# Kernel optimization log

Hardware: AMD Instinct MI355X
Metric: run time of the kernel (lower is better)

## Reference

```python
import jax, jax.numpy as jnp
import numpy as np

EPS = 1e-5          # BatchNorm eps
SG_ALPHA = 4.0      # spikingjelly sigmoid surrogate alpha
NUM_EXPERTS = 8
TOP_K = 2
ROUTER_TAU = 2.0
TAUS = tuple(1.5 + (4.0 - 1.5) * i / (NUM_EXPERTS - 1) for i in range(NUM_EXPERTS))

@jax.custom_vjp
def spike(x):
    # Heaviside(x >= 0) with sigmoid surrogate gradient
    return (x >= 0).astype(x.dtype)

def _spike_fwd(x):
    return spike(x), x

def _spike_bwd(x, g):
    s = jax.nn.sigmoid(SG_ALPHA * x)
    return (g * SG_ALPHA * s * (1.0 - s),)

spike.defvjp(_spike_fwd, _spike_bwd)

def conv1x1(x, w, b):
    # x: (N,C,H,W), w: (O,C) 1x1 conv kernel, b: (O,)
    return jnp.einsum('nchw,oc->nohw', x, w) + b[None, :, None, None]

def bn(x, gamma, beta):
    # fresh BatchNorm2d inference: running_mean=0, running_var=1
    scale = gamma / np.float32(np.sqrt(1.0 + EPS))
    return x * scale[None, :, None, None] + beta[None, :, None, None]

def setup_inputs() -> dict:
    key = jax.random.key(0)
    ks = jax.random.split(key, 16)
    T, B, C, H, W = 4, 64, 64, 32, 32
    E = NUM_EXPERTS
    inp = {
        'x':  jax.random.normal(ks[0], (T, B, C, H, W), jnp.float32) * 2.0,
        'w1': jax.random.normal(ks[1], (E, C, C), jnp.float32) * 0.05,
        'b1': jax.random.normal(ks[2], (E, C), jnp.float32) * 0.05,
        'g1': jax.random.uniform(ks[3], (E, C), jnp.float32, 0.5, 1.5),
        'be1': jax.random.normal(ks[4], (E, C), jnp.float32) * 0.05,
        'w2': jax.random.normal(ks[5], (E, C, C), jnp.float32) * 0.05,
        'b2': jax.random.normal(ks[6], (E, C), jnp.float32) * 0.05,
        'g2': jax.random.uniform(ks[7], (E, C), jnp.float32, 0.5, 1.5),
        'be2': jax.random.normal(ks[8], (E, C), jnp.float32) * 0.05,
        'rw': jax.random.normal(ks[9], (E, C), jnp.float32) * 0.05,
        'rb': jax.random.normal(ks[10], (E,), jnp.float32) * 0.05,
        'rg': jax.random.uniform(ks[11], (E,), jnp.float32, 0.5, 1.5),
        'rbe': jax.random.normal(ks[12], (E,), jnp.float32) * 0.05,
    }
    return inp

def reference(x, w1, b1, g1, be1, w2, b2, g2, be2, rw, rb, rg, rbe):
    T, B, C, H, W = x.shape
    N = T * B
    # ---- Router: multi-step LIF over T, then 1x1 conv + BN + spatial mean ----
    def lif_step(v, xt):
        v = v + (xt - v) / ROUTER_TAU
        s = spike(v - 1.0)
        v = v * (1.0 - jax.lax.stop_gradient(s))  # detach_reset, hard reset to 0
        return v, s
    _, spk = jax.lax.scan(lif_step, jnp.zeros_like(x[0]), x)  # (T,B,C,H,W)
    r = bn(conv1x1(spk.reshape(N, C, H, W), rw, rb), rg, rbe)  # (N,E,H,W)
    logits = r.mean(axis=(2, 3))                               # (N,E)
    probs = jax.nn.softmax(logits, axis=-1)
    wk, idx = jax.lax.top_k(probs, TOP_K)                      # (N,k)
    wk = wk / wk.sum(axis=-1, keepdims=True)
    wk = jax.lax.stop_gradient(wk)                             # weights detached
    # dense combine weights: weight of expert e for each token (0 if unselected)
    combine = jnp.zeros((N, NUM_EXPERTS), x.dtype).at[jnp.arange(N)[:, None], idx].add(wk)
    # ---- Experts: each token processed independently (T=1, fresh LIF state) ----
    xf = x.reshape(N, C, H, W)
    out = jnp.zeros_like(xf)
    for e in range(NUM_EXPERTS):
        tau = TAUS[e]
        s1 = spike(xf / tau - 1.0)                 # single-step LIF: v=x/tau, thresh 1
        h = bn(conv1x1(s1, w1[e], b1[e]), g1[e], be1[e])
        x2 = xf + h                                # res=True (hidden == in_features)
        s2 = spike(x2 / tau - 1.0)
        y = bn(conv1x1(s2, w2[e], b2[e]), g2[e], be2[e])
        eo = y + x2                                # expert's own residual
        out = out + combine[:, e, None, None, None] * eo
    return (out + xf).reshape(T, B, C, H, W)       # final identity add
```

## Files before the change

kernel.cpp:

```cpp
#include <hip/hip_runtime.h>
#include <hip/hip_bf16.h>

#define TT 4
#define BB 64
#define CC 64
#define PP 1024
#define NN 256
#define EE 8

#define RSQ 0.99999500003749975f

typedef __attribute__((ext_vector_type(8))) short short8;
typedef __attribute__((ext_vector_type(4))) float f32x4;

static __device__ __forceinline__ float rfl_f(float v) {
    return __uint_as_float(__builtin_amdgcn_readfirstlane(__float_as_uint(v)));
}
static __device__ __forceinline__ unsigned short f2bf(float v) {
    __hip_bfloat16 h = __float2bfloat16(v);
    return *reinterpret_cast<unsigned short*>(&h);
}

__global__ void k_lif_prep(const float* __restrict__ x, float* __restrict__ mean_spk,
                           const float* __restrict__ w1, const float* __restrict__ b1,
                           const float* __restrict__ g1, const float* __restrict__ be1,
                           const float* __restrict__ w2, const float* __restrict__ b2,
                           const float* __restrict__ g2, const float* __restrict__ be2,
                           unsigned short* __restrict__ wb,
                           float* __restrict__ fb1, float* __restrict__ fb2) {
    if (blockIdx.x >= BB * CC) {
        int idx = (blockIdx.x - BB * CC) * 256 + threadIdx.x;
        if (idx < EE * CC * CC) {
            int e = idx >> 12, rem = idx & 4095;
            int o = rem >> 6;
            float s1 = g1[e * 64 + o] * RSQ;
            float s2 = g2[e * 64 + o] * RSQ;
            wb[(e * 2 + 0) * 4096 + rem] = f2bf(w1[idx] * s1);
            wb[(e * 2 + 1) * 4096 + rem] = f2bf(w2[idx] * s2);
        }
        if (idx < EE * CC) {
            fb1[idx] = b1[idx] * (g1[idx] * RSQ) + be1[idx];
            fb2[idx] = b2[idx] * (g2[idx] * RSQ) + be2[idx];
        }
        return;
    }
    int bc = blockIdx.x;
    int b = bc >> 6, c = bc & 63;
    int tid = threadIdx.x;
    const size_t tstride = (size_t)BB * CC * PP;
    const float* xp = x + ((size_t)b * CC + c) * PP + tid * 4;
    f32x4 v = {0.f, 0.f, 0.f, 0.f};
    float cnt[4];
    #pragma unroll
    for (int t = 0; t < 4; ++t) {
        f32x4 xt = *(const f32x4*)(xp + t * tstride);
        float cc = 0.f;
        #pragma unroll
        for (int r = 0; r < 4; ++r) {
            v[r] += (xt[r] - v[r]) * 0.5f;
            bool s = v[r] >= 1.f;
            cc += s ? 1.f : 0.f;
            v[r] = s ? 0.f : v[r];
        }
        cnt[t] = cc;
    }
    __shared__ float red[4][4];
    int lane = tid & 63, wv = tid >> 6;
    #pragma unroll
    for (int off = 32; off > 0; off >>= 1) {
        cnt[0] += __shfl_down(cnt[0], off, 64);
        cnt[1] += __shfl_down(cnt[1], off, 64);
        cnt[2] += __shfl_down(cnt[2], off, 64);
        cnt[3] += __shfl_down(cnt[3], off, 64);
    }
    if (lane == 0) { red[wv][0] = cnt[0]; red[wv][1] = cnt[1]; red[wv][2] = cnt[2]; red[wv][3] = cnt[3]; }
    __syncthreads();
    if (tid < 4) {
        float s = red[0][tid] + red[1][tid] + red[2][tid] + red[3][tid];
        mean_spk[((size_t)tid * BB + b) * CC + c] = s * (1.f / 1024.f);
    }
}

template <int BIT>
static __device__ __forceinline__ short8 unpack8(unsigned d0, unsigned d1) {
    const unsigned am = 0x00010001u << BIT;
    const unsigned mu = 0x3F80u >> BIT;
    union { unsigned u[4]; short8 s; } cv;
    unsigned t;
    t = __builtin_amdgcn_perm(0u, d0, 0x0C010C00u) & am; cv.u[0] = t * mu;
    t = __builtin_amdgcn_perm(0u, d0, 0x0C030C02u) & am; cv.u[1] = t * mu;
    t = __builtin_amdgcn_perm(0u, d1, 0x0C010C00u) & am; cv.u[2] = t * mu;
    t = __builtin_amdgcn_perm(0u, d1, 0x0C030C02u) & am; cv.u[3] = t * mu;
    return cv.s;
}

__global__ void __launch_bounds__(256) __attribute__((amdgpu_waves_per_eu(4, 8))) k_experts(
    const float* __restrict__ x, const float* __restrict__ mean_spk,
    const float* __restrict__ rw, const float* __restrict__ rb,
    const float* __restrict__ rg, const float* __restrict__ rbe,
    const unsigned short* __restrict__ wb,
    const float* __restrict__ fb1, const float* __restrict__ fb2,
    float* __restrict__ out)
{
    __shared__ unsigned char s1[2][64 * 72];
    __shared__ unsigned char s2[2][64 * 72];

    int blk = blockIdx.x;
    int n = blk >> 2;
    int q = blk & 3;
    int tid = threadIdx.x;
    int z = tid >> 6;
    int lane = tid & 63;
    int l16 = lane & 15;
    int g = lane >> 4;
    int Q0 = q << 8;
    int ch = z * 16 + l16;

    const float* __restrict__ xn = x + (size_t)n * (CC * PP);

    int re = lane >> 3, rcb = (lane & 7) << 3;
    f32x4 msv0 = *(const f32x4*)(mean_spk + n * CC + rcb);
    f32x4 msv1 = *(const f32x4*)(mean_spk + n * CC + rcb + 4);
    f32x4 rwv0 = *(const f32x4*)(rw + re * CC + rcb);
    f32x4 rwv1 = *(const f32x4*)(rw + re * CC + rcb + 4);

    f32x4 xsbuf[2][4];
    {
        const float* xc = xn + (size_t)ch * PP + Q0 + 4 * g;
        #pragma unroll
        for (int tm = 0; tm < 4; ++tm)
            xsbuf[0][tm] = *(const f32x4*)(xc + tm * 16);
    }

    float part = 0.f;
    #pragma unroll
    for (int r = 0; r < 4; ++r) part = fmaf(msv0[r], rwv0[r], part);
    #pragma unroll
    for (int r = 0; r < 4; ++r) part = fmaf(msv1[r], rwv1[r], part);
    part += __shfl_xor(part, 1, 64);
    part += __shfl_xor(part, 2, 64);
    part += __shfl_xor(part, 4, 64);
    float logit = (part + rb[re]) * (rg[re] * RSQ) + rbe[re];
    float l[EE];
    #pragma unroll
    for (int j = 0; j < EE; ++j) l[j] = __shfl(logit, j << 3, 64);
    float m = l[0];
    #pragma unroll
    for (int e = 1; e < EE; ++e) m = fmaxf(m, l[e]);
    float pr[EE];
    #pragma unroll
    for (int e = 0; e < EE; ++e) pr[e] = __expf(l[e] - m);
    int e1i = 0; float v1 = pr[0];
    #pragma unroll
    for (int e = 1; e < EE; ++e) { if (pr[e] > v1) { v1 = pr[e]; e1i = e; } }
    int e2i = (e1i == 0) ? 1 : 0; float v2 = (e1i == 0) ? pr[1] : pr[0];
    #pragma unroll
    for (int e = 0; e < EE; ++e) { if (e != e1i && pr[e] > v2) { v2 = pr[e]; e2i = e; } }
    float wAv = v1 / (v1 + v2), wBv = v2 / (v1 + v2);

    int e1 = __builtin_amdgcn_readfirstlane(e1i);
    int e2 = __builtin_amdgcn_readfirstlane(e2i);
    wAv = rfl_f(wAv); wBv = rfl_f(wBv);
    float tauA = (float)(1.5 + 2.5 * (double)e1 / 7.0);
    float tauB = (float)(1.5 + 2.5 * (double)e2 / 7.0);
    float kx = (1.f + wAv + wBv) / wAv;

    const unsigned short* wbA = wb + e1 * 8192;
    const unsigned short* wbB = wb + e2 * 8192;

    short8 w1A[2], w1B[2], w2A[2], w2B[2];
    #pragma unroll
    for (int ks = 0; ks < 2; ++ks) {
        int wo = ch * 64 + ks * 32 + g * 8;
        w1A[ks] = *(const short8*)(wbA + wo);
        w1B[ks] = *(const short8*)(wbB + wo);
        w2A[ks] = *(const short8*)(wbA + 4096 + wo);
        w2B[ks] = *(const short8*)(wbB + 4096 + wo);
    }
    float b1A = fb1[e1 * 64 + ch];
    float b1B = fb1[e2 * 64 + ch];
    float cst = wAv * fb2[e1 * 64 + ch] + wBv * fb2[e2 * 64 + ch];

    #pragma unroll
    for (int tm = 0; tm < 4; ++tm)
        #pragma unroll
        for (int r = 0; r < 4; ++r) {
            float xv = xsbuf[0][tm][r];
            s1[0][(tm * 16 + 4 * g + r) * 72 + ch] =
                (unsigned char)((xv >= tauA ? 1u : 0u) | (xv >= tauB ? 2u : 0u));
        }
    __syncthreads();

    float* __restrict__ on = out + (size_t)n * (CC * PP);

    #pragma unroll
    for (int s = 0; s < 4; ++s) {
        const int par = s & 1, nxt = par ^ 1;

        if (s < 3) {
            const float* xc = xn + (size_t)ch * PP + Q0 + (s + 1) * 64 + 4 * g;
            #pragma unroll
            for (int tm = 0; tm < 4; ++tm)
                xsbuf[nxt][tm] = *(const f32x4*)(xc + tm * 16);
        }

        f32x4 accA[4], accB[4];
        #pragma unroll
        for (int tm = 0; tm < 4; ++tm) {
            accA[tm] = (f32x4){0.f, 0.f, 0.f, 0.f};
            accB[tm] = (f32x4){0.f, 0.f, 0.f, 0.f};
        }
        #pragma unroll
        for (int ks = 0; ks < 2; ++ks)
            #pragma unroll
            for (int tm = 0; tm < 4; ++tm) {
                const unsigned* mp = (const unsigned*)(&s1[par][0] + (tm * 16 + l16) * 72 + ks * 32 + g * 8);
                unsigned d0 = mp[0], d1 = mp[1];
                short8 aA = unpack8<0>(d0, d1);
                accA[tm] = __builtin_amdgcn_mfma_f32_16x16x32_bf16(aA, w1A[ks], accA[tm], 0, 0, 0);
                short8 aB = unpack8<1>(d0, d1);
                accB[tm] = __builtin_amdgcn_mfma_f32_16x16x32_bf16(aB, w1B[ks], accB[tm], 0, 0, 0);
            }

        #pragma unroll
        for (int tm = 0; tm < 4; ++tm)
            #pragma unroll
            for (int r = 0; r < 4; ++r) {
                float xv = xsbuf[par][tm][r];
                float bnA = accA[tm][r] + b1A;
                float bnB = accB[tm][r] + b1B;
                s2[par][(tm * 16 + 4 * g + r) * 72 + ch] =
                    (unsigned char)(((xv + bnA) >= tauA ? 1u : 0u) | ((xv + bnB) >= tauB ? 2u : 0u));
                accA[tm][r] = fmaf(xv, kx, bnA);
                accB[tm][r] = bnB;
            }

        if (s < 3) {
            #pragma unroll
            for (int tm = 0; tm < 4; ++tm)
                #pragma unroll
                for (int r = 0; r < 4; ++r) {
                    float xv = xsbuf[nxt][tm][r];
                    s1[nxt][(tm * 16 + 4 * g + r) * 72 + ch] =
                        (unsigned char)((xv >= tauA ? 1u : 0u) | (xv >= tauB ? 2u : 0u));
                }
        }
        __syncthreads();

        #pragma unroll
        for (int ks = 0; ks < 2; ++ks)
            #pragma unroll
            for (int tm = 0; tm < 4; ++tm) {
                const unsigned* mp = (const unsigned*)(&s2[par][0] + (tm * 16 + l16) * 72 + ks * 32 + g * 8);
                unsigned d0 = mp[0], d1 = mp[1];
                short8 aA = unpack8<0>(d0, d1);
                accA[tm] = __builtin_amdgcn_mfma_f32_16x16x32_bf16(aA, w2A[ks], accA[tm], 0, 0, 0);
                short8 aB = unpack8<1>(d0, d1);
                accB[tm] = __builtin_amdgcn_mfma_f32_16x16x32_bf16(aB, w2B[ks], accB[tm], 0, 0, 0);
            }

        #pragma unroll
        for (int tm = 0; tm < 4; ++tm) {
            f32x4 o;
            #pragma unroll
            for (int r = 0; r < 4; ++r)
                o[r] = fmaf(wAv, accA[tm][r], fmaf(wBv, accB[tm][r], cst));
            *(f32x4*)(on + (size_t)ch * PP + Q0 + s * 64 + tm * 16 + 4 * g) = o;
        }
    }
}

extern "C" void kernel_launch(void* const* d_in, const int* in_sizes, int n_in,
                              void* d_out, int out_size, void* d_ws, size_t ws_size,
                              hipStream_t stream) {
    const float* x   = (const float*)d_in[0];
    const float* w1  = (const float*)d_in[1];
    const float* b1  = (const float*)d_in[2];
    const float* g1  = (const float*)d_in[3];
    const float* be1 = (const float*)d_in[4];
    const float* w2  = (const float*)d_in[5];
    const float* b2  = (const float*)d_in[6];
    const float* g2  = (const float*)d_in[7];
    const float* be2 = (const float*)d_in[8];
    const float* rw  = (const float*)d_in[9];
    const float* rb  = (const float*)d_in[10];
    const float* rg  = (const float*)d_in[11];
    const float* rbe = (const float*)d_in[12];
    float* out = (float*)d_out;
    float* ws  = (float*)d_ws;

    float* mean_spk     = ws;
    unsigned short* wb  = (unsigned short*)(ws + 16384);
    float* fb1          = ws + 49152;
    float* fb2          = ws + 49664;

    hipLaunchKernelGGL(k_lif_prep, dim3(BB * CC + 128), dim3(256), 0, stream,
                       x, mean_spk, w1, b1, g1, be1, w2, b2, g2, be2, wb, fb1, fb2);
    hipLaunchKernelGGL(k_experts, dim3(NN * 4), dim3(256), 0, stream,
                       x, mean_spk, rw, rb, rg, rbe, wb, fb1, fb2, out);
}
```

Before: 48.70 us.

## Store spike masks as bf16 in LDS instead of packed bytes

Spike masks now go into shared memory as bf16 values (0 or 1.0) in separate per-expert planes, where before they were packed bits in bytes. The MFMA operands are then loaded directly as short8 with no perm/and/mul unpacking. Bias b1 is folded into the accumulator init, and an extra barrier is added because the s1 and s2 buffers are no longer double-buffered per stage. In exchange the LDS footprint and store traffic double per element, and the extra barrier adds synchronisation in each stage.

```diff
diff --git a/kernel.cpp b/kernel.cpp
--- a/kernel.cpp
+++ b/kernel.cpp
@@ -81,19 +81,6 @@
     }
 }
 
-template <int BIT>
-static __device__ __forceinline__ short8 unpack8(unsigned d0, unsigned d1) {
-    const unsigned am = 0x00010001u << BIT;
-    const unsigned mu = 0x3F80u >> BIT;
-    union { unsigned u[4]; short8 s; } cv;
-    unsigned t;
-    t = __builtin_amdgcn_perm(0u, d0, 0x0C010C00u) & am; cv.u[0] = t * mu;
-    t = __builtin_amdgcn_perm(0u, d0, 0x0C030C02u) & am; cv.u[1] = t * mu;
-    t = __builtin_amdgcn_perm(0u, d1, 0x0C010C00u) & am; cv.u[2] = t * mu;
-    t = __builtin_amdgcn_perm(0u, d1, 0x0C030C02u) & am; cv.u[3] = t * mu;
-    return cv.s;
-}
-
 __global__ void __launch_bounds__(256) __attribute__((amdgpu_waves_per_eu(4, 8))) k_experts(
     const float* __restrict__ x, const float* __restrict__ mean_spk,
     const float* __restrict__ rw, const float* __restrict__ rb,
@@ -102,8 +89,8 @@
     const float* __restrict__ fb1, const float* __restrict__ fb2,
     float* __restrict__ out)
 {
-    __shared__ unsigned char s1[2][64 * 72];
-    __shared__ unsigned char s2[2][64 * 72];
+    __shared__ unsigned short s1p[2][64 * 72];
+    __shared__ unsigned short s2p[2][64 * 72];
 
     int blk = blockIdx.x;
     int n = blk >> 2;
@@ -186,8 +173,9 @@
         #pragma unroll
         for (int r = 0; r < 4; ++r) {
             float xv = xsbuf[0][tm][r];
-            s1[0][(tm * 16 + 4 * g + r) * 72 + ch] =
-                (unsigned char)((xv >= tauA ? 1u : 0u) | (xv >= tauB ? 2u : 0u));
+            int px = tm * 16 + 4 * g + r;
+            s1p[0][px * 72 + ch] = (xv >= tauA) ? (unsigned short)0x3F80 : (unsigned short)0;
+            s1p[1][px * 72 + ch] = (xv >= tauB) ? (unsigned short)0x3F80 : (unsigned short)0;
         }
     __syncthreads();
 
@@ -207,32 +195,32 @@
         f32x4 accA[4], accB[4];
         #pragma unroll
         for (int tm = 0; tm < 4; ++tm) {
-            accA[tm] = (f32x4){0.f, 0.f, 0.f, 0.f};
-            accB[tm] = (f32x4){0.f, 0.f, 0.f, 0.f};
+            accA[tm] = (f32x4){b1A, b1A, b1A, b1A};
+            accB[tm] = (f32x4){b1B, b1B, b1B, b1B};
         }
         #pragma unroll
         for (int ks = 0; ks < 2; ++ks)
             #pragma unroll
             for (int tm = 0; tm < 4; ++tm) {
-                const unsigned* mp = (const unsigned*)(&s1[par][0] + (tm * 16 + l16) * 72 + ks * 32 + g * 8);
-                unsigned d0 = mp[0], d1 = mp[1];
-                short8 aA = unpack8<0>(d0, d1);
+                const unsigned short* rowp = &s1p[0][(tm * 16 + l16) * 72 + ks * 32 + g * 8];
+                short8 aA = *(const short8*)rowp;
+                short8 aB = *(const short8*)(rowp + 64 * 72);
                 accA[tm] = __builtin_amdgcn_mfma_f32_16x16x32_bf16(aA, w1A[ks], accA[tm], 0, 0, 0);
-                short8 aB = unpack8<1>(d0, d1);
                 accB[tm] = __builtin_amdgcn_mfma_f32_16x16x32_bf16(aB, w1B[ks], accB[tm], 0, 0, 0);
             }
+        __syncthreads();
 
         #pragma unroll
         for (int tm = 0; tm < 4; ++tm)
             #pragma unroll
             for (int r = 0; r < 4; ++r) {
                 float xv = xsbuf[par][tm][r];
-                float bnA = accA[tm][r] + b1A;
-                float bnB = accB[tm][r] + b1B;
-                s2[par][(tm * 16 + 4 * g + r) * 72 + ch] =
-                    (unsigned char)(((xv + bnA) >= tauA ? 1u : 0u) | ((xv + bnB) >= tauB ? 2u : 0u));
+                float bnA = accA[tm][r];
+                float bnB = accB[tm][r];
+                int px = tm * 16 + 4 * g + r;
+                s2p[0][px * 72 + ch] = ((xv + bnA) >= tauA) ? (unsigned short)0x3F80 : (unsigned short)0;
+                s2p[1][px * 72 + ch] = ((xv + bnB) >= tauB) ? (unsigned short)0x3F80 : (unsigned short)0;
                 accA[tm][r] = fmaf(xv, kx, bnA);
-                accB[tm][r] = bnB;
             }
 
         if (s < 3) {
@@ -241,8 +229,9 @@
                 #pragma unroll
                 for (int r = 0; r < 4; ++r) {
                     float xv = xsbuf[nxt][tm][r];
-                    s1[nxt][(tm * 16 + 4 * g + r) * 72 + ch] =
-                        (unsigned char)((xv >= tauA ? 1u : 0u) | (xv >= tauB ? 2u : 0u));
+                    int px = tm * 16 + 4 * g + r;
+                    s1p[0][px * 72 + ch] = (xv >= tauA) ? (unsigned short)0x3F80 : (unsigned short)0;
+                    s1p[1][px * 72 + ch] = (xv >= tauB) ? (unsigned short)0x3F80 : (unsigned short)0;
                 }
         }
         __syncthreads();
@@ -251,11 +240,10 @@
         for (int ks = 0; ks < 2; ++ks)
             #pragma unroll
             for (int tm = 0; tm < 4; ++tm) {
-                const unsigned* mp = (const unsigned*)(&s2[par][0] + (tm * 16 + l16) * 72 + ks * 32 + g * 8);
-                unsigned d0 = mp[0], d1 = mp[1];
-                short8 aA = unpack8<0>(d0, d1);
+                const unsigned short* rowp = &s2p[0][(tm * 16 + l16) * 72 + ks * 32 + g * 8];
+                short8 aA = *(const short8*)rowp;
+                short8 aB = *(const short8*)(rowp + 64 * 72);
                 accA[tm] = __builtin_amdgcn_mfma_f32_16x16x32_bf16(aA, w2A[ks], accA[tm], 0, 0, 0);
-                short8 aB = unpack8<1>(d0, d1);
                 accB[tm] = __builtin_amdgcn_mfma_f32_16x16x32_bf16(aB, w2B[ks], accB[tm], 0, 0, 0);
             }
 
```

After: 46.71 us (median of 2 runs). 1.04x faster.

## Fuse LIF router prep and expert phase into one cooperative kernel with grid sync

Applied to the files above, without the earlier changes.

Merges the LIF/weight-prep kernel and the expert kernel into a single cooperative launch of 1024 blocks. Each block first does four (b,c) LIF reductions plus a share of weight prep, then waits at a grid-wide sync before running the expert phase. This removes a kernel launch and the gap between the two kernels. The cost is a grid barrier, and the launch falls back to two kernels if the grid cannot be co-resident. The change also drops the LDS double buffering in favour of single buffers with an extra __syncthreads, and folds b1 into the accumulator initialisation.

```diff
diff --git a/kernel.cpp b/kernel.cpp
--- a/kernel.cpp
+++ b/kernel.cpp
@@ -1,5 +1,6 @@
 #include <hip/hip_runtime.h>
 #include <hip/hip_bf16.h>
+#include <hip/hip_cooperative_groups.h>
 
 #define TT 4
 #define BB 64
@@ -13,12 +14,27 @@
 typedef __attribute__((ext_vector_type(8))) short short8;
 typedef __attribute__((ext_vector_type(4))) float f32x4;
 
+namespace cg = cooperative_groups;
+
 static __device__ __forceinline__ float rfl_f(float v) {
     return __uint_as_float(__builtin_amdgcn_readfirstlane(__float_as_uint(v)));
 }
 static __device__ __forceinline__ unsigned short f2bf(float v) {
     __hip_bfloat16 h = __float2bfloat16(v);
     return *reinterpret_cast<unsigned short*>(&h);
+}
+
+template <int BIT>
+static __device__ __forceinline__ short8 unpack8(unsigned d0, unsigned d1) {
+    const unsigned am = 0x00010001u << BIT;
+    const unsigned mu = 0x3F80u >> BIT;
+    union { unsigned u[4]; short8 s; } cv;
+    unsigned t;
+    t = __builtin_amdgcn_perm(0u, d0, 0x0C010C00u) & am; cv.u[0] = t * mu;
+    t = __builtin_amdgcn_perm(0u, d0, 0x0C030C02u) & am; cv.u[1] = t * mu;
+    t = __builtin_amdgcn_perm(0u, d1, 0x0C010C00u) & am; cv.u[2] = t * mu;
+    t = __builtin_amdgcn_perm(0u, d1, 0x0C030C02u) & am; cv.u[3] = t * mu;
+    return cv.s;
 }
 
 __global__ void k_lif_prep(const float* __restrict__ x, float* __restrict__ mean_spk,
@@ -81,17 +97,177 @@
     }
 }
 
-template <int BIT>
-static __device__ __forceinline__ short8 unpack8(unsigned d0, unsigned d1) {
-    const unsigned am = 0x00010001u << BIT;
-    const unsigned mu = 0x3F80u >> BIT;
-    union { unsigned u[4]; short8 s; } cv;
-    unsigned t;
-    t = __builtin_amdgcn_perm(0u, d0, 0x0C010C00u) & am; cv.u[0] = t * mu;
-    t = __builtin_amdgcn_perm(0u, d0, 0x0C030C02u) & am; cv.u[1] = t * mu;
-    t = __builtin_amdgcn_perm(0u, d1, 0x0C010C00u) & am; cv.u[2] = t * mu;
-    t = __builtin_amdgcn_perm(0u, d1, 0x0C030C02u) & am; cv.u[3] = t * mu;
-    return cv.s;
+static __device__ __forceinline__ void expert_phase(
+    int blk, int tid,
+    const float* __restrict__ x, const float* __restrict__ mean_spk,
+    const float* __restrict__ rw, const float* __restrict__ rb,
+    const float* __restrict__ rg, const float* __restrict__ rbe,
+    const unsigned short* __restrict__ wb,
+    const float* __restrict__ fb1, const float* __restrict__ fb2,
+    float* __restrict__ out,
+    unsigned char* __restrict__ s1, unsigned char* __restrict__ s2)
+{
+    int n = blk >> 2;
+    int q = blk & 3;
+    int z = tid >> 6;
+    int lane = tid & 63;
+    int l16 = lane & 15;
+    int g = lane >> 4;
+    int Q0 = q << 8;
+    int ch = z * 16 + l16;
+
+    const float* __restrict__ xn = x + (size_t)n * (CC * PP);
+
+    int re = lane >> 3, rcb = (lane & 7) << 3;
+    f32x4 msv0 = *(const f32x4*)(mean_spk + n * CC + rcb);
+    f32x4 msv1 = *(const f32x4*)(mean_spk + n * CC + rcb + 4);
+    f32x4 rwv0 = *(const f32x4*)(rw + re * CC + rcb);
+    f32x4 rwv1 = *(const f32x4*)(rw + re * CC + rcb + 4);
+
+    f32x4 xsbuf[2][4];
+    {
+        const float* xc = xn + (size_t)ch * PP + Q0 + 4 * g;
+        #pragma unroll
+        for (int tm = 0; tm < 4; ++tm)
+            xsbuf[0][tm] = *(const f32x4*)(xc + tm * 16);
+    }
+
+    float part = 0.f;
+    #pragma unroll
+    for (int r = 0; r < 4; ++r) part = fmaf(msv0[r], rwv0[r], part);
+    #pragma unroll
+    for (int r = 0; r < 4; ++r) part = fmaf(msv1[r], rwv1[r], part);
+    part += __shfl_xor(part, 1, 64);
+    part += __shfl_xor(part, 2, 64);
+    part += __shfl_xor(part, 4, 64);
+    float logit = (part + rb[re]) * (rg[re] * RSQ) + rbe[re];
+    float l[EE];
+    #pragma unroll
+    for (int j = 0; j < EE; ++j) l[j] = __shfl(logit, j << 3, 64);
+    float m = l[0];
+    #pragma unroll
+    for (int e = 1; e < EE; ++e) m = fmaxf(m, l[e]);
+    float pr[EE];
+    #pragma unroll
+    for (int e = 0; e < EE; ++e) pr[e] = __expf(l[e] - m);
+    int e1i = 0; float v1 = pr[0];
+    #pragma unroll
+    for (int e = 1; e < EE; ++e) { if (pr[e] > v1) { v1 = pr[e]; e1i = e; } }
+    int e2i = (e1i == 0) ? 1 : 0; float v2 = (e1i == 0) ? pr[1] : pr[0];
+    #pragma unroll
+    for (int e = 0; e < EE; ++e) { if (e != e1i && pr[e] > v2) { v2 = pr[e]; e2i = e; } }
+    float wAv = v1 / (v1 + v2), wBv = v2 / (v1 + v2);
+
+    int e1 = __builtin_amdgcn_readfirstlane(e1i);
+    int e2 = __builtin_amdgcn_readfirstlane(e2i);
+    wAv = rfl_f(wAv); wBv = rfl_f(wBv);
+    float tauA = (float)(1.5 + 2.5 * (double)e1 / 7.0);
+    float tauB = (float)(1.5 + 2.5 * (double)e2 / 7.0);
+    float kx = (1.f + wAv + wBv) / wAv;
+
+    const unsigned short* wbA = wb + e1 * 8192;
+    const unsigned short* wbB = wb + e2 * 8192;
+
+    short8 w1A[2], w1B[2], w2A[2], w2B[2];
+    #pragma unroll
+    for (int ks = 0; ks < 2; ++ks) {
+        int wo = ch * 64 + ks * 32 + g * 8;
+        w1A[ks] = *(const short8*)(wbA + wo);
+        w1B[ks] = *(const short8*)(wbB + wo);
+        w2A[ks] = *(const short8*)(wbA + 4096 + wo);
+        w2B[ks] = *(const short8*)(wbB + 4096 + wo);
+    }
+    float b1A = fb1[e1 * 64 + ch];
+    float b1B = fb1[e2 * 64 + ch];
+    float cst = wAv * fb2[e1 * 64 + ch] + wBv * fb2[e2 * 64 + ch];
+
+    #pragma unroll
+    for (int tm = 0; tm < 4; ++tm)
+        #pragma unroll
+        for (int r = 0; r < 4; ++r) {
+            float xv = xsbuf[0][tm][r];
+            s1[(tm * 16 + 4 * g + r) * 72 + ch] =
+                (unsigned char)((xv >= tauA ? 1u : 0u) | (xv >= tauB ? 2u : 0u));
+        }
+    __syncthreads();
+
+    float* __restrict__ on = out + (size_t)n * (CC * PP);
+
+    #pragma unroll
+    for (int s = 0; s < 4; ++s) {
+        const int par = s & 1, nxt = par ^ 1;
+
+        if (s < 3) {
+            const float* xc = xn + (size_t)ch * PP + Q0 + (s + 1) * 64 + 4 * g;
+            #pragma unroll
+            for (int tm = 0; tm < 4; ++tm)
+                xsbuf[nxt][tm] = *(const f32x4*)(xc + tm * 16);
+        }
+
+        f32x4 accA[4], accB[4];
+        #pragma unroll
+        for (int tm = 0; tm < 4; ++tm) {
+            accA[tm] = (f32x4){b1A, b1A, b1A, b1A};
+            accB[tm] = (f32x4){b1B, b1B, b1B, b1B};
+        }
+        #pragma unroll
+        for (int ks = 0; ks < 2; ++ks)
+            #pragma unroll
+            for (int tm = 0; tm < 4; ++tm) {
+                const unsigned* mp = (const unsigned*)(s1 + (tm * 16 + l16) * 72 + ks * 32 + g * 8);
+                unsigned d0 = mp[0], d1 = mp[1];
+                short8 aA = unpack8<0>(d0, d1);
+                accA[tm] = __builtin_amdgcn_mfma_f32_16x16x32_bf16(aA, w1A[ks], accA[tm], 0, 0, 0);
+                short8 aB = unpack8<1>(d0, d1);
+                accB[tm] = __builtin_amdgcn_mfma_f32_16x16x32_bf16(aB, w1B[ks], accB[tm], 0, 0, 0);
+            }
+        __syncthreads();
+
+        #pragma unroll
+        for (int tm = 0; tm < 4; ++tm)
+            #pragma unroll
+            for (int r = 0; r < 4; ++r) {
+                float xv = xsbuf[par][tm][r];
+                float bnA = accA[tm][r];
+                float bnB = accB[tm][r];
+                s2[(tm * 16 + 4 * g + r) * 72 + ch] =
+                    (unsigned char)(((xv + bnA) >= tauA ? 1u : 0u) | ((xv + bnB) >= tauB ? 2u : 0u));
+                accA[tm][r] = fmaf(xv, kx, bnA);
+            }
+
+        if (s < 3) {
+            #pragma unroll
+            for (int tm = 0; tm < 4; ++tm)
+                #pragma unroll
+                for (int r = 0; r < 4; ++r) {
+                    float xv = xsbuf[nxt][tm][r];
+                    s1[(tm * 16 + 4 * g + r) * 72 + ch] =
+                        (unsigned char)((xv >= tauA ? 1u : 0u) | (xv >= tauB ? 2u : 0u));
+                }
+        }
+        __syncthreads();
+
+        #pragma unroll
+        for (int ks = 0; ks < 2; ++ks)
+            #pragma unroll
+            for (int tm = 0; tm < 4; ++tm) {
+                const unsigned* mp = (const unsigned*)(s2 + (tm * 16 + l16) * 72 + ks * 32 + g * 8);
+                unsigned d0 = mp[0], d1 = mp[1];
+                short8 aA = unpack8<0>(d0, d1);
+                accA[tm] = __builtin_amdgcn_mfma_f32_16x16x32_bf16(aA, w2A[ks], accA[tm], 0, 0, 0);
+                short8 aB = unpack8<1>(d0, d1);
+                accB[tm] = __builtin_amdgcn_mfma_f32_16x16x32_bf16(aB, w2B[ks], accB[tm], 0, 0, 0);
+            }
+
+        #pragma unroll
+        for (int tm = 0; tm < 4; ++tm) {
+            f32x4 o;
+            #pragma unroll
+            for (int r = 0; r < 4; ++r)
+                o[r] = fmaf(wAv, accA[tm][r], fmaf(wBv, accB[tm][r], cst));
+            *(f32x4*)(on + (size_t)ch * PP + Q0 + s * 64 + tm * 16 + 4 * g) = o;
+        }
+    }
 }
 
 __global__ void __launch_bounds__(256) __attribute__((amdgpu_waves_per_eu(4, 8))) k_experts(
@@ -102,172 +278,89 @@
     const float* __restrict__ fb1, const float* __restrict__ fb2,
     float* __restrict__ out)
 {
-    __shared__ unsigned char s1[2][64 * 72];
-    __shared__ unsigned char s2[2][64 * 72];
+    __shared__ unsigned char s1[64 * 72];
+    __shared__ unsigned char s2[64 * 72];
+    expert_phase(blockIdx.x, threadIdx.x, x, mean_spk, rw, rb, rg, rbe,
+                 wb, fb1, fb2, out, s1, s2);
+}
+
+__global__ void __launch_bounds__(256) __attribute__((amdgpu_waves_per_eu(4, 8))) k_fused(
+    const float* __restrict__ x,
+    const float* __restrict__ w1, const float* __restrict__ b1,
+    const float* __restrict__ g1, const float* __restrict__ be1,
+    const float* __restrict__ w2, const float* __restrict__ b2,
+    const float* __restrict__ g2, const float* __restrict__ be2,
+    const float* __restrict__ rw, const float* __restrict__ rb,
+    const float* __restrict__ rg, const float* __restrict__ rbe,
+    float* __restrict__ mean_spk, unsigned short* __restrict__ wb,
+    float* __restrict__ fb1, float* __restrict__ fb2,
+    float* __restrict__ out)
+{
+    __shared__ unsigned char s1[64 * 72];
+    __shared__ unsigned char s2[64 * 72];
+    __shared__ float red[4][4];
 
     int blk = blockIdx.x;
-    int n = blk >> 2;
-    int q = blk & 3;
     int tid = threadIdx.x;
-    int z = tid >> 6;
     int lane = tid & 63;
-    int l16 = lane & 15;
-    int g = lane >> 4;
-    int Q0 = q << 8;
-    int ch = z * 16 + l16;
-
-    const float* __restrict__ xn = x + (size_t)n * (CC * PP);
-
-    int re = lane >> 3, rcb = (lane & 7) << 3;
-    f32x4 msv0 = *(const f32x4*)(mean_spk + n * CC + rcb);
-    f32x4 msv1 = *(const f32x4*)(mean_spk + n * CC + rcb + 4);
-    f32x4 rwv0 = *(const f32x4*)(rw + re * CC + rcb);
-    f32x4 rwv1 = *(const f32x4*)(rw + re * CC + rcb + 4);
-
-    f32x4 xsbuf[2][4];
-    {
-        const float* xc = xn + (size_t)ch * PP + Q0 + 4 * g;
-        #pragma unroll
-        for (int tm = 0; tm < 4; ++tm)
-            xsbuf[0][tm] = *(const f32x4*)(xc + tm * 16);
-    }
-
-    float part = 0.f;
-    #pragma unroll
-    for (int r = 0; r < 4; ++r) part = fmaf(msv0[r], rwv0[r], part);
-    #pragma unroll
-    for (int r = 0; r < 4; ++r) part = fmaf(msv1[r], rwv1[r], part);
-    part += __shfl_xor(part, 1, 64);
-    part += __shfl_xor(part, 2, 64);
-    part += __shfl_xor(part, 4, 64);
-    float logit = (part + rb[re]) * (rg[re] * RSQ) + rbe[re];
-    float l[EE];
-    #pragma unroll
-    for (int j = 0; j < EE; ++j) l[j] = __shfl(logit, j << 3, 64);
-    float m = l[0];
-    #pragma unroll
-    for (int e = 1; e < EE; ++e) m = fmaxf(m, l[e]);
-    float pr[EE];
-    #pragma unroll
-    for (int e = 0; e < EE; ++e) pr[e] = __expf(l[e] - m);
-    int e1i = 0; float v1 = pr[0];
-    #pragma unroll
-    for (int e = 1; e < EE; ++e) { if (pr[e] > v1) { v1 = pr[e]; e1i = e; } }
-    int e2i = (e1i == 0) ? 1 : 0; float v2 = (e1i == 0) ? pr[1] : pr[0];
-    #pragma unroll
-    for (int e = 0; e < EE; ++e) { if (e != e1i && pr[e] > v2) { v2 = pr[e]; e2i = e; } }
-    float wAv = v1 / (v1 + v2), wBv = v2 / (v1 + v2);
-
-    int e1 = __builtin_amdgcn_readfirstlane(e1i);
-    int e2 = __builtin_amdgcn_readfirstlane(e2i);
-    wAv = rfl_f(wAv); wBv = rfl_f(wBv);
-    float tauA = (float)(1.5 + 2.5 * (double)e1 / 7.0);
-    float tauB = (float)(1.5 + 2.5 * (double)e2 / 7.0);
-    float kx = (1.f + wAv + wBv) / wAv;
-
-    const unsigned short* wbA = wb + e1 * 8192;
-    const unsigned short* wbB = wb + e2 * 8192;
-
-    short8 w1A[2], w1B[2], w2A[2], w2B[2];
-    #pragma unroll
-    for (int ks = 0; ks < 2; ++ks) {
-        int wo = ch * 64 + ks * 32 + g * 8;
-        w1A[ks] = *(const short8*)(wbA + wo);
-        w1B[ks] = *(const short8*)(wbB + wo);
-        w2A[ks] = *(const short8*)(wbA + 4096 + wo);
-        w2B[ks] = *(const short8*)(wbB + 4096 + wo);
-    }
-    float b1A = fb1[e1 * 64 + ch];
-    float b1B = fb1[e2 * 64 + ch];
-    float cst = wAv * fb2[e1 * 64 + ch] + wBv * fb2[e2 * 64 + ch];
-
-    #pragma unroll
-    for (int tm = 0; tm < 4; ++tm)
-        #pragma unroll
-        for (int r = 0; r < 4; ++r) {
-            float xv = xsbuf[0][tm][r];
-            s1[0][(tm * 16 + 4 * g + r) * 72 + ch] =
-                (unsigned char)((xv >= tauA ? 1u : 0u) | (xv >= tauB ? 2u : 0u));
-        }
-    __syncthreads();
-
-    float* __restrict__ on = out + (size_t)n * (CC * PP);
-
-    #pragma unroll
-    for (int s = 0; s < 4; ++s) {
-        const int par = s & 1, nxt = par ^ 1;
-
-        if (s < 3) {
-            const float* xc = xn + (size_t)ch * PP + Q0 + (s + 1) * 64 + 4 * g;
-            #pragma unroll
-            for (int tm = 0; tm < 4; ++tm)
-                xsbuf[nxt][tm] = *(const f32x4*)(xc + tm * 16);
-        }
-
-        f32x4 accA[4], accB[4];
-        #pragma unroll
-        for (int tm = 0; tm < 4; ++tm) {
-            accA[tm] = (f32x4){0.f, 0.f, 0.f, 0.f};
-            accB[tm] = (f32x4){0.f, 0.f, 0.f, 0.f};
-        }
-        #pragma unroll
-        for (int ks = 0; ks < 2; ++ks)
-            #pragma unroll
-            for (int tm = 0; tm < 4; ++tm) {
-                const unsigned* mp = (const unsigned*)(&s1[par][0] + (tm * 16 + l16) * 72 + ks * 32 + g * 8);
-                unsigned d0 = mp[0], d1 = mp[1];
-                short8 aA = unpack8<0>(d0, d1);
-                accA[tm] = __builtin_amdgcn_mfma_f32_16x16x32_bf16(aA, w1A[ks], accA[tm], 0, 0, 0);
-                short8 aB = unpack8<1>(d0, d1);
-                accB[tm] = __builtin_amdgcn_mfma_f32_16x16x32_bf16(aB, w1B[ks], accB[tm], 0, 0, 0);
+    int wv = tid >> 6;
+
+    if (blk < 128) {
+        int idx = blk * 256 + tid;
+        int e = idx >> 12, rem = idx & 4095;
+        int o = rem >> 6;
+        float sA = g1[e * 64 + o] * RSQ;
+        float sB = g2[e * 64 + o] * RSQ;
+        wb[(e * 2 + 0) * 4096 + rem] = f2bf(w1[idx] * sA);
+        wb[(e * 2 + 1) * 4096 + rem] = f2bf(w2[idx] * sB);
+        if (idx < EE * CC) {
+            fb1[idx] = b1[idx] * (g1[idx] * RSQ) + be1[idx];
+            fb2[idx] = b2[idx] * (g2[idx] * RSQ) + be2[idx];
+        }
+    }
+
+    const size_t tstride = (size_t)BB * CC * PP;
+    #pragma unroll
+    for (int k = 0; k < 4; ++k) {
+        int bc = blk * 4 + k;
+        int b = bc >> 6, c = bc & 63;
+        const float* xp = x + ((size_t)b * CC + c) * PP + tid * 4;
+        f32x4 v = {0.f, 0.f, 0.f, 0.f};
+        float cnt[4];
+        #pragma unroll
+        for (int t = 0; t < 4; ++t) {
+            f32x4 xt = *(const f32x4*)(xp + t * tstride);
+            float cc = 0.f;
+            #pragma unroll
+            for (int r = 0; r < 4; ++r) {
+                v[r] += (xt[r] - v[r]) * 0.5f;
+                bool s = v[r] >= 1.f;
+                cc += s ? 1.f : 0.f;
+                v[r] = s ? 0.f : v[r];
             }
-
-        #pragma unroll
-        for (int tm = 0; tm < 4; ++tm)
-            #pragma unroll
-            for (int r = 0; r < 4; ++r) {
-                float xv = xsbuf[par][tm][r];
-                float bnA = accA[tm][r] + b1A;
-                float bnB = accB[tm][r] + b1B;
-                s2[par][(tm * 16 + 4 * g + r) * 72 + ch] =
-                    (unsigned char)(((xv + bnA) >= tauA ? 1u : 0u) | ((xv + bnB) >= tauB ? 2u : 0u));
-                accA[tm][r] = fmaf(xv, kx, bnA);
-                accB[tm][r] = bnB;
-            }
-
-        if (s < 3) {
-            #pragma unroll
-            for (int tm = 0; tm < 4; ++tm)
-                #pragma unroll
-                for (int r = 0; r < 4; ++r) {
-                    float xv = xsbuf[nxt][tm][r];
-                    s1[nxt][(tm * 16 + 4 * g + r) * 72 + ch] =
-                        (unsigned char)((xv >= tauA ? 1u : 0u) | (xv >= tauB ? 2u : 0u));
-                }
-        }
+            cnt[t] = cc;
+        }
+        #pragma unroll
+        for (int off = 32; off > 0; off >>= 1) {
+            cnt[0] += __shfl_down(cnt[0], off, 64);
+            cnt[1] += __shfl_down(cnt[1], off, 64);
+            cnt[2] += __shfl_down(cnt[2], off, 64);
+            cnt[3] += __shfl_down(cnt[3], off, 64);
+        }
+        if (lane == 0) { red[wv][0] = cnt[0]; red[wv][1] = cnt[1]; red[wv][2] = cnt[2]; red[wv][3] = cnt[3]; }
         __syncthreads();
-
-        #pragma unroll
-        for (int ks = 0; ks < 2; ++ks)
-            #pragma unroll
-            for (int tm = 0; tm < 4; ++tm) {
-                const unsigned* mp = (const unsigned*)(&s2[par][0] + (tm * 16 + l16) * 72 + ks * 32 + g * 8);
-                unsigned d0 = mp[0], d1 = mp[1];
-                short8 aA = unpack8<0>(d0, d1);
-                accA[tm] = __builtin_amdgcn_mfma_f32_16x16x32_bf16(aA, w2A[ks], accA[tm], 0, 0, 0);
-                short8 aB = unpack8<1>(d0, d1);
-                accB[tm] = __builtin_amdgcn_mfma_f32_16x16x32_bf16(aB, w2B[ks], accB[tm], 0, 0, 0);
-            }
-
-        #pragma unroll
-        for (int tm = 0; tm < 4; ++tm) {
-            f32x4 o;
-            #pragma unroll
-            for (int r = 0; r < 4; ++r)
-                o[r] = fmaf(wAv, accA[tm][r], fmaf(wBv, accB[tm][r], cst));
-            *(f32x4*)(on + (size_t)ch * PP + Q0 + s * 64 + tm * 16 + 4 * g) = o;
-        }
-    }
+        if (tid < 4) {
+            float s = red[0][tid] + red[1][tid] + red[2][tid] + red[3][tid];
+            mean_spk[((size_t)tid * BB + b) * CC + c] = s * (1.f / 1024.f);
+        }
+        __syncthreads();
+    }
+
+    __threadfence();
+    cg::this_grid().sync();
+    __threadfence();
+
+    expert_phase(blk, tid, x, mean_spk, rw, rb, rg, rbe, wb, fb1, fb2, out, s1, s2);
 }
 
 extern "C" void kernel_launch(void* const* d_in, const int* in_sizes, int n_in,
@@ -294,6 +387,27 @@
     float* fb1          = ws + 49152;
     float* fb2          = ws + 49664;
 
+    bool coop_ok = false;
+    int dev = 0, numCU = 0, maxBlk = 0;
+    if (hipGetDevice(&dev) == hipSuccess &&
+        hipDeviceGetAttribute(&numCU, hipDeviceAttributeMultiprocessorCount, dev) == hipSuccess &&
+        hipOccupancyMaxActiveBlocksPerMultiprocessor(&maxBlk, (const void*)k_fused, 256, 0) == hipSuccess) {
+        coop_ok = ((long long)maxBlk * numCU >= NN * 4);
+    }
+
+    if (coop_ok) {
+        void* args[] = {
+            (void*)&x, (void*)&w1, (void*)&b1, (void*)&g1, (void*)&be1,
+            (void*)&w2, (void*)&b2, (void*)&g2, (void*)&be2,
+            (void*)&rw, (void*)&rb, (void*)&rg, (void*)&rbe,
+            (void*)&mean_spk, (void*)&wb, (void*)&fb1, (void*)&fb2, (void*)&out
+        };
+        hipError_t err = hipLaunchCooperativeKernel((const void*)k_fused,
+                                                    dim3(NN * 4), dim3(256),
+                                                    args, 0, stream);
+        if (err == hipSuccess) return;
+    }
+
     hipLaunchKernelGGL(k_lif_prep, dim3(BB * CC + 128), dim3(256), 0, stream,
                        x, mean_spk, w1, b1, g1, be1, w2, b2, g2, be2, wb, fb1, fb2);
     hipLaunchKernelGGL(k_experts, dim3(NN * 4), dim3(256), 0, stream,
```

Result: slower. 54.52 us (+11.9%).
